# Performance work log

Hardware: AMD Instinct MI355X
Metric: run time of the kernel (lower is better)

The kernel has to match this reference:

```python
import jax, jax.numpy as jnp
import numpy as np

DIM = 1024
NUM_HEADS = 16
HEAD_DIM = DIM // NUM_HEADS


def setup_inputs() -> dict:
    key = jax.random.key(0)
    ks = jax.random.split(key, 5)
    B, T = 2, 2048
    x = jax.random.normal(ks[0], (B, T, DIM), dtype=jnp.float32)
    s = 1.0 / np.sqrt(DIM)
    W_qkv = jax.random.normal(ks[1], (DIM, 3 * DIM), dtype=jnp.float32) * s
    b_qkv = jnp.zeros((3 * DIM,), dtype=jnp.float32)
    W_out = jax.random.normal(ks[2], (DIM, DIM), dtype=jnp.float32) * s
    b_out = jnp.zeros((DIM,), dtype=jnp.float32)
    return {"x": x, "W_qkv": W_qkv, "b_qkv": b_qkv, "W_out": W_out, "b_out": b_out}


def reference(x, W_qkv, b_qkv, W_out, b_out):
    B, T, D = x.shape
    H, Hd = NUM_HEADS, HEAD_DIM
    qkv = x @ W_qkv + b_qkv                       # [B,T,3D]
    qkv = qkv.reshape(B, T, 3, H, Hd)
    q = jnp.transpose(qkv[:, :, 0], (0, 2, 1, 3))  # [B,H,T,Hd]
    k = jnp.transpose(qkv[:, :, 1], (0, 2, 1, 3))
    v = jnp.transpose(qkv[:, :, 2], (0, 2, 1, 3))
    att = jnp.einsum('bhqd,bhkd->bhqk', q, k) / np.sqrt(Hd)  # [B,H,T,T]
    causal = jnp.tril(jnp.ones((T, T), dtype=bool))
    att = jnp.where(causal[None, None], att, -jnp.inf)
    att = jax.nn.softmax(att, axis=-1)
    out = jnp.einsum('bhqk,bhkd->bhqd', att, v)   # [B,H,T,Hd]
    out = jnp.transpose(out, (0, 2, 1, 3)).reshape(B, T, D)
    return out @ W_out + b_out
```

## Files before the change

kernel.cpp:

```cpp
#include <hip/hip_runtime.h>
#include <hip/hip_bf16.h>

typedef unsigned short u16;
typedef __attribute__((ext_vector_type(8))) short short8;
typedef __attribute__((ext_vector_type(4))) float f32x4;
typedef __attribute__((ext_vector_type(4))) unsigned short u16x4;

#define LOG2E 1.44269504088896340736f


__device__ __forceinline__ void gl_lds16(const void* g, void* l) {
  __builtin_amdgcn_global_load_lds(
      (__attribute__((address_space(1))) void*)g,
      (__attribute__((address_space(3))) void*)l, 16, 0, 0);
}

__device__ __forceinline__ float exp2_fast(float x) {
#if __has_builtin(__builtin_amdgcn_exp2f)
  return __builtin_amdgcn_exp2f(x);
#else
  return exp2f(x);
#endif
}

__device__ __forceinline__ u16 f2bf(float f) {
  union { float f; unsigned int i; } v;
  v.f = f;
  unsigned int r = v.i + 0x7fffu + ((v.i >> 16) & 1u);
  return (u16)(r >> 16);
}

__device__ __forceinline__ unsigned int pack_bf2(float lo, float hi) {
  union { __hip_bfloat162 h2; unsigned int u; } c;
  c.h2 = __float22bfloat162_rn(make_float2(lo, hi));
  return c.u;
}


__global__ __launch_bounds__(256) void prep_kernel(
    const float4* __restrict__ x, u16x4* __restrict__ xb,
    const float* __restrict__ Wqkv, u16* __restrict__ WqkvT,
    const float* __restrict__ Wout, u16* __restrict__ WoutT) {
  __shared__ u16 t[64][65];
  int bid = blockIdx.x, tid = threadIdx.x;
  if (bid < 4096) {
    int i = bid * 256 + tid;
    float4 v = x[i];
    u16x4 o;
    o.x = f2bf(v.x); o.y = f2bf(v.y); o.z = f2bf(v.z); o.w = f2bf(v.w);
    xb[i] = o;
    return;
  }
  const float* W;
  u16* WT;
  int K = 1024, N, bxx, byy;
  if (bid < 4864) {
    int tt = bid - 4096;
    W = Wqkv; WT = WqkvT; N = 3072; bxx = tt % 48; byy = tt / 48;
  } else {
    int tt = bid - 4864;
    W = Wout; WT = WoutT; N = 1024; bxx = tt % 16; byy = tt / 16;
  }
  int r0 = byy * 64, c0 = bxx * 64;
  int tx = tid & 63, ty = tid >> 6;
  for (int r = ty; r < 64; r += 4)
    t[r][tx] = f2bf(W[(size_t)(r0 + r) * N + c0 + tx]);
  __syncthreads();
  for (int r = ty; r < 64; r += 4)
    WT[(size_t)(c0 + r) * K + r0 + tx] = t[tx][r];
}


template <bool OUT_F32, int BN>
__global__ __launch_bounds__(256) void gemm_bt_kernel(
    const u16* __restrict__ A, const u16* __restrict__ Bt,
    const float* __restrict__ bias, void* __restrict__ Cout,
    int M, int N, int K) {
  constexpr int NBJ = BN / 32;
  constexpr int CH_A = 16;
  constexpr int CH_B = BN / 8;
  constexpr int PER_W = (CH_A + CH_B) / 4;
  __shared__ u16 As[128 * 64];
  __shared__ u16 Bs[BN * 64];
  int tid = threadIdx.x;
  int w = tid >> 6, lane = tid & 63, l15 = lane & 15, quad = lane >> 4;
  int m0 = blockIdx.y * 128, n0 = blockIdx.x * BN;
  int wm = (w & 1) * 64, wn = (w >> 1) * (BN / 2);

  f32x4 acc[4][NBJ];
#pragma unroll
  for (int i = 0; i < 4; ++i)
#pragma unroll
    for (int j = 0; j < NBJ; ++j) {
      f32x4 z = {0.f, 0.f, 0.f, 0.f};
      acc[i][j] = z;
    }

  int r8 = lane >> 3;
  int sw = ((lane & 7) ^ r8) * 8;

  for (int kt = 0; kt < K; kt += 64) {
    __syncthreads();
#pragma unroll
    for (int i = 0; i < PER_W; ++i) {
      int c = w * PER_W + i;
      if (c < CH_A) {
        int row = m0 + c * 8 + r8;
        gl_lds16(A + (size_t)row * K + kt + sw, As + c * 512);
      } else {
        int cc = c - CH_A;
        int row = n0 + cc * 8 + r8;
        gl_lds16(Bt + (size_t)row * K + kt + sw, Bs + cc * 512);
      }
    }
    __syncthreads();

#pragma unroll
    for (int kh = 0; kh < 2; ++kh) {
      short8 af[4], bf[NBJ];
#pragma unroll
      for (int i = 0; i < 4; ++i) {
        int R = wm + i * 16 + l15;
        af[i] = *(const short8*)(As + R * 64 +
                                 ((kh * 32 + quad * 8) ^ ((R & 7) * 8)));
      }
#pragma unroll
      for (int j = 0; j < NBJ; ++j) {
        int R = wn + j * 16 + l15;
        bf[j] = *(const short8*)(Bs + R * 64 +
                                 ((kh * 32 + quad * 8) ^ ((R & 7) * 8)));
      }
#pragma unroll
      for (int i = 0; i < 4; ++i)
#pragma unroll
        for (int j = 0; j < NBJ; ++j)
          acc[i][j] = __builtin_amdgcn_mfma_f32_16x16x32_bf16(af[i], bf[j],
                                                              acc[i][j], 0, 0, 0);
    }
  }

  float bv[NBJ];
#pragma unroll
  for (int j = 0; j < NBJ; ++j) bv[j] = bias[n0 + wn + j * 16 + l15];
#pragma unroll
  for (int i = 0; i < 4; ++i)
#pragma unroll
    for (int j = 0; j < NBJ; ++j) {
      int col = n0 + wn + j * 16 + l15;
#pragma unroll
      for (int r = 0; r < 4; ++r) {
        int row = m0 + wm + i * 16 + quad * 4 + r;
        float val = acc[i][j][r] + bv[j];
        if (OUT_F32)
          ((float*)Cout)[(size_t)row * N + col] = val;
        else
          ((u16*)Cout)[(size_t)row * N + col] = f2bf(val);
      }
    }
}


__global__ __launch_bounds__(512, 2) void flash_kernel(
    const u16* __restrict__ qkv, u16* __restrict__ att) {
  __shared__ unsigned int SH[28672];

  int tid = threadIdx.x;
  int w = tid >> 6, half = w >> 2, wq = w & 3;
  int lane = tid & 63, l15 = lane & 15, quad = lane >> 4;
  int bx = blockIdx.x;
  int p = bx >> 5, bh = bx & 31, b = bh >> 4, h = bh & 15;
  const int qs[2] = {15 - p, p};
  const int kmax0 = 2 * qs[0] + 1, kmax1 = 2 * p + 1;
  const int jmax = 16 - p;

  const u16* base = qkv + (size_t)b * 2048 * 3072 + h * 64;
  const u16* kb = base + 1024;
  const u16* vb = base + 2048;

  int ht = tid & 255;
  const int krow = ht >> 3, h7 = ht & 7;
  const int swk = (h7 ^ (krow & 7)) * 8;

  short8 qf[2][2][2];
#pragma unroll
  for (int t = 0; t < 2; ++t) {
    const u16* qtb = base + (size_t)(qs[t] * 128 + wq * 32 + l15) * 3072;
    qf[t][0][0] = *(const short8*)(qtb + quad * 8);
    qf[t][0][1] = *(const short8*)(qtb + 32 + quad * 8);
    qf[t][1][0] = *(const short8*)(qtb + 16 * 3072 + quad * 8);
    qf[t][1][1] = *(const short8*)(qtb + 16 * 3072 + 32 + quad * 8);
  }

  {
    unsigned int* Ks0 = SH + half * 2048;
    gl_lds16(kb + (size_t)(half * 64 + krow) * 3072 + swk,
             (char*)Ks0 + wq * 1024);
    gl_lds16(kb + (size_t)(half * 64 + 32 + krow) * 3072 + swk,
             (char*)Ks0 + 4096 + wq * 1024);
  }
  uint4 vr0 = *(const uint4*)(vb + (size_t)(half * 64 + 2 * krow) * 3072 + h7 * 8);
  uint4 vr1 = *(const uint4*)(vb + (size_t)(half * 64 + 2 * krow + 1) * 3072 + h7 * 8);

  f32x4 o[2][2][4];
#pragma unroll
  for (int t = 0; t < 2; ++t)
#pragma unroll
    for (int qsub = 0; qsub < 2; ++qsub)
#pragma unroll
      for (int jd = 0; jd < 4; ++jd) {
        f32x4 z = {0.f, 0.f, 0.f, 0.f};
        o[t][qsub][jd] = z;
      }
  float lsum[2][2] = {0.f, 0.f, 0.f, 0.f};

  const int psw = (l15 & 7) << 2;
  const float kscale = 0.125f * LOG2E;
  unsigned int* Pw = SH + 20480 + w * 1024;

  int b3 = 0;
  for (int j = 0; j < jmax; ++j) {
    int kt = 2 * j + half;
    unsigned int* KsH = SH + b3 * 4096 + half * 2048;
    unsigned int* VtH = SH + 12288 + (j & 1) * 4096 + half * 2048;

    {
      const u16* av = (const u16*)&vr0;
      const u16* bvp = (const u16*)&vr1;
#pragma unroll
      for (int jj = 0; jj < 8; ++jj) {
        int d = h7 * 8 + jj;
        VtH[32 * d + (krow ^ ((jj ^ h7) << 2))] =
            (unsigned int)av[jj] | ((unsigned int)bvp[jj] << 16);
      }
    }

    int nb3 = b3 + 1;
    if (nb3 == 3) nb3 = 0;
    if (j + 1 < jmax) {
      int kn = (kt + 2) * 64;
      unsigned int* Ksn = SH + nb3 * 4096 + half * 2048;
      gl_lds16(kb + (size_t)(kn + krow) * 3072 + swk, (char*)Ksn + wq * 1024);
      gl_lds16(kb + (size_t)(kn + 32 + krow) * 3072 + swk,
               (char*)Ksn + 4096 + wq * 1024);
      vr0 = *(const uint4*)(vb + (size_t)(kn + 2 * krow) * 3072 + h7 * 8);
      vr1 = *(const uint4*)(vb + (size_t)(kn + 2 * krow + 1) * 3072 + h7 * 8);
    }
    b3 = nb3;

    asm volatile("s_waitcnt lgkmcnt(0)" ::: "memory");
    __builtin_amdgcn_s_barrier();
    asm volatile("" ::: "memory");

#pragma unroll
    for (int t = 0; t < 2; ++t) {
      int km = t ? kmax1 : kmax0;
      if (kt > km) continue;
      bool last = (kt == km);
      if (last && wq < 2) continue;
      bool domask = last || ((kt == km - 1) && wq < 2);
      int qloc = ((last ? (wq - 2) : wq) << 5) + l15;

      f32x4 s0[4], s1[4];
#pragma unroll
      for (int jn = 0; jn < 4; ++jn) {
        f32x4 z = {0.f, 0.f, 0.f, 0.f};
        s0[jn] = z;
        s1[jn] = z;
      }
#pragma unroll
      for (int ss = 0; ss < 2; ++ss) {
        short8 a0 = qf[t][0][ss];
        short8 a1 = qf[t][1][ss];
#pragma unroll
        for (int jn = 0; jn < 4; ++jn) {
          int row = jn * 16 + l15;
          short8 bk = *(const short8*)&KsH[32 * row + ((16 * ss + 4 * quad) ^
                                                       ((row & 7) << 2))];
          s0[jn] = __builtin_amdgcn_mfma_f32_16x16x32_bf16(bk, a0, s0[jn], 0, 0, 0);
          s1[jn] = __builtin_amdgcn_mfma_f32_16x16x32_bf16(bk, a1, s1[jn], 0, 0, 0);
        }
      }

#pragma unroll
      for (int qsub = 0; qsub < 2; ++qsub) {
        int qq = qloc + qsub * 16;
        float ls = 0.f;
#pragma unroll
        for (int jn = 0; jn < 4; ++jn) {
          f32x4 sv = qsub ? s1[jn] : s0[jn];
          float pv[4];
#pragma unroll
          for (int r = 0; r < 4; ++r) {
            float e = exp2_fast(fmaf(sv[r], kscale, -16.0f));
            if (domask && (jn * 16 + quad * 4 + r > qq)) e = 0.f;
            pv[r] = e;
            ls += e;
          }
          uint2 dd = make_uint2(pack_bf2(pv[0], pv[1]), pack_bf2(pv[2], pv[3]));
          *(uint2*)&Pw[qsub * 512 + 32 * l15 +
                       (((jn << 3) + (quad << 1)) ^ psw)] = dd;
        }
        lsum[t][qsub] += ls;
      }

#pragma unroll
      for (int ss = 0; ss < 2; ++ss) {
        short8 pf0 = *(const short8*)&Pw[32 * l15 +
                                         (((ss << 4) + (quad << 2)) ^ psw)];
        short8 pf1 = *(const short8*)&Pw[512 + 32 * l15 +
                                         (((ss << 4) + (quad << 2)) ^ psw)];
#pragma unroll
        for (int jd = 0; jd < 4; ++jd) {
          int vrow = jd * 16 + l15;
          int f = (vrow & 7) ^ ((vrow >> 3) & 7);
          short8 bvv = *(const short8*)&VtH[32 * vrow +
                                            (((ss << 4) + (quad << 2)) ^ (f << 2))];
          o[t][0][jd] =
              __builtin_amdgcn_mfma_f32_16x16x32_bf16(bvv, pf0, o[t][0][jd], 0, 0, 0);
          o[t][1][jd] =
              __builtin_amdgcn_mfma_f32_16x16x32_bf16(bvv, pf1, o[t][1][jd], 0, 0, 0);
        }
      }
    }
  }

  float lf[2][2];
#pragma unroll
  for (int t = 0; t < 2; ++t)
#pragma unroll
    for (int qsub = 0; qsub < 2; ++qsub) {
      float v = lsum[t][qsub];
      v += __shfl_xor(v, 16, 64);
      v += __shfl_xor(v, 32, 64);
      lf[t][qsub] = v;
    }

  float* OM = (float*)SH;
  float* LM = (float*)(SH + 8704);
  __syncthreads();
#pragma unroll
  for (int t = 0; t < 2; ++t) {
    if (half == 0) {
#pragma unroll
      for (int qsub = 0; qsub < 2; ++qsub) {
        int q = wq * 32 + qsub * 16 + l15;
#pragma unroll
        for (int jd = 0; jd < 4; ++jd)
          *(float4*)&OM[q * 68 + jd * 16 + quad * 4] = *(float4*)&o[t][qsub][jd];
        if (quad == 0) LM[q] = lf[t][qsub];
      }
    }
    __syncthreads();
    if (half == 1) {
#pragma unroll
      for (int qsub = 0; qsub < 2; ++qsub) {
        int q = wq * 32 + qsub * 16 + l15;
        float lr = lf[t][qsub] + LM[q];
        float inv = 1.f / lr;
        size_t row = (size_t)b * 2048 + qs[t] * 128 + q;
        u16* orow = att + row * 1024 + h * 64 + quad * 4;
#pragma unroll
        for (int jd = 0; jd < 4; ++jd) {
          float4 pa = *(float4*)&OM[q * 68 + jd * 16 + quad * 4];
          uint2 dd = make_uint2(pack_bf2((o[t][qsub][jd][0] + pa.x) * inv,
                                         (o[t][qsub][jd][1] + pa.y) * inv),
                                pack_bf2((o[t][qsub][jd][2] + pa.z) * inv,
                                         (o[t][qsub][jd][3] + pa.w) * inv));
          *(uint2*)(orow + jd * 16) = dd;
        }
      }
    }
    __syncthreads();
  }
}


extern "C" void kernel_launch(void* const* d_in, const int* in_sizes, int n_in,
                              void* d_out, int out_size, void* d_ws,
                              size_t ws_size, hipStream_t stream) {
  const float* x = (const float*)d_in[0];
  const float* Wqkv = (const float*)d_in[1];
  const float* bqkv = (const float*)d_in[2];
  const float* Wout = (const float*)d_in[3];
  const float* bout = (const float*)d_in[4];
  float* out = (float*)d_out;

  char* ws = (char*)d_ws;
  u16* WqkvT = (u16*)(ws);
  u16* WoutT = (u16*)(ws + 6291456);
  u16* qkv = (u16*)(ws + 8388608);
  u16* attn = (u16*)(ws + 33554432);
  u16* xb = (u16*)(ws + 41943040);

  prep_kernel<<<5120, 256, 0, stream>>>((const float4*)x, (u16x4*)xb, Wqkv,
                                        WqkvT, Wout, WoutT);
  gemm_bt_kernel<false, 128><<<dim3(24, 32), 256, 0, stream>>>(
      xb, WqkvT, bqkv, (void*)qkv, 4096, 3072, 1024);
  flash_kernel<<<256, 512, 0, stream>>>(qkv, attn);
  gemm_bt_kernel<true, 64><<<dim3(16, 32), 256, 0, stream>>>(
      attn, WoutT, bout, (void*)out, 4096, 1024, 1024);
}
```

Baseline: 169.4 us.

## Use 256x256-tile 8-wave GEMM kernel for QKV projection

Adds a new GEMM kernel with 256x256 output tiles, 8 waves each computing 128x64, and double-buffered LDS filled by direct global-to-LDS loads with XOR swizzle. It is used for the QKV projection in place of the 128-wide tile kernel. Larger tiles raise data reuse and cut global traffic per FLOP. The cost is a grid of only 192 blocks on a GPU with many CUs, one block per CU, and a full vmcnt(0) wait plus barrier every K step, which limits latency hiding.

```diff
diff --git a/kernel.cpp b/kernel.cpp
--- a/kernel.cpp
+++ b/kernel.cpp
@@ -160,6 +160,101 @@
 }
 
 
+template <bool OUT_F32>
+__global__ __launch_bounds__(512, 1) void gemm8_kernel(
+    const u16* __restrict__ A, const u16* __restrict__ Bt,
+    const float* __restrict__ bias, void* __restrict__ Cout,
+    int M, int N, int K) {
+  __shared__ u16 LDS[2][2][256 * 64];
+  int tid = threadIdx.x;
+  int w = tid >> 6, lane = tid & 63, l15 = lane & 15, quad = lane >> 4;
+  int m0 = blockIdx.y * 256, n0 = blockIdx.x * 256;
+  int wm = (w & 1) * 128, wn = (w >> 1) * 64;
+
+  f32x4 acc[8][4];
+#pragma unroll
+  for (int i = 0; i < 8; ++i)
+#pragma unroll
+    for (int j = 0; j < 4; ++j) {
+      f32x4 z = {0.f, 0.f, 0.f, 0.f};
+      acc[i][j] = z;
+    }
+
+  int r8 = lane >> 3;
+  int sw = ((lane & 7) ^ r8) * 8;
+
+  const u16* Asrc = A + (size_t)(m0 + w * 32 + r8) * K + sw;
+  const u16* Bsrc = Bt + (size_t)(n0 + w * 32 + r8) * K + sw;
+  int nt = K >> 6;
+
+#pragma unroll
+  for (int i = 0; i < 4; ++i) {
+    gl_lds16(Asrc + (size_t)(i * 8) * K, &LDS[0][0][(w * 4 + i) * 512]);
+    gl_lds16(Bsrc + (size_t)(i * 8) * K, &LDS[0][1][(w * 4 + i) * 512]);
+  }
+
+  for (int t = 0; t < nt; ++t) {
+    asm volatile("s_waitcnt vmcnt(0)" ::: "memory");
+    __builtin_amdgcn_s_barrier();
+    asm volatile("" ::: "memory");
+    int cur = t & 1;
+    if (t + 1 < nt) {
+      int koff = (t + 1) << 6;
+#pragma unroll
+      for (int i = 0; i < 4; ++i) {
+        gl_lds16(Asrc + (size_t)(i * 8) * K + koff,
+                 &LDS[cur ^ 1][0][(w * 4 + i) * 512]);
+        gl_lds16(Bsrc + (size_t)(i * 8) * K + koff,
+                 &LDS[cur ^ 1][1][(w * 4 + i) * 512]);
+      }
+    }
+    const u16* As = &LDS[cur][0][0];
+    const u16* Bs = &LDS[cur][1][0];
+#pragma unroll
+    for (int kh = 0; kh < 2; ++kh) {
+      short8 af[8], bf[4];
+#pragma unroll
+      for (int i = 0; i < 8; ++i) {
+        int R = wm + i * 16 + l15;
+        af[i] = *(const short8*)(As + R * 64 +
+                                 ((kh * 32 + quad * 8) ^ ((R & 7) * 8)));
+      }
+#pragma unroll
+      for (int j = 0; j < 4; ++j) {
+        int R = wn + j * 16 + l15;
+        bf[j] = *(const short8*)(Bs + R * 64 +
+                                 ((kh * 32 + quad * 8) ^ ((R & 7) * 8)));
+      }
+#pragma unroll
+      for (int i = 0; i < 8; ++i)
+#pragma unroll
+        for (int j = 0; j < 4; ++j)
+          acc[i][j] = __builtin_amdgcn_mfma_f32_16x16x32_bf16(af[i], bf[j],
+                                                              acc[i][j], 0, 0, 0);
+    }
+  }
+
+  float bv[4];
+#pragma unroll
+  for (int j = 0; j < 4; ++j) bv[j] = bias[n0 + wn + j * 16 + l15];
+#pragma unroll
+  for (int i = 0; i < 8; ++i)
+#pragma unroll
+    for (int j = 0; j < 4; ++j) {
+      int col = n0 + wn + j * 16 + l15;
+#pragma unroll
+      for (int r = 0; r < 4; ++r) {
+        int row = m0 + wm + i * 16 + quad * 4 + r;
+        float val = acc[i][j][r] + bv[j];
+        if (OUT_F32)
+          ((float*)Cout)[(size_t)row * N + col] = val;
+        else
+          ((u16*)Cout)[(size_t)row * N + col] = f2bf(val);
+      }
+    }
+}
+
+
 __global__ __launch_bounds__(512, 2) void flash_kernel(
     const u16* __restrict__ qkv, u16* __restrict__ att) {
   __shared__ unsigned int SH[28672];
@@ -394,7 +489,7 @@
 
   prep_kernel<<<5120, 256, 0, stream>>>((const float4*)x, (u16x4*)xb, Wqkv,
                                         WqkvT, Wout, WoutT);
-  gemm_bt_kernel<false, 128><<<dim3(24, 32), 256, 0, stream>>>(
+  gemm8_kernel<false><<<dim3(12, 16), 512, 0, stream>>>(
       xb, WqkvT, bqkv, (void*)qkv, 4096, 3072, 1024);
   flash_kernel<<<256, 512, 0, stream>>>(qkv, attn);
   gemm_bt_kernel<true, 64><<<dim3(16, 32), 256, 0, stream>>>(
```

After: 173.2 us. 2.3% more time.

## Double-buffer GEMM LDS loads with 8-wave blocks and larger tiles

Applied to the files above, without the earlier changes.

Replaces the 4-wave GEMM with an 8-wave kernel that double-buffers the A/B tiles in LDS. The next K-tile's global-to-LDS loads are issued before the current tile's MFMAs, and the second barrier per iteration is removed. Tiles grow to 256x192 for the QKV projection and 128x128 for the output projection, which launches 256 blocks per GEMM. This aims to hide load latency and improve data reuse, but it raises register and LDS use and may leave CUs underfilled.

```diff
diff --git a/kernel.cpp b/kernel.cpp
--- a/kernel.cpp
+++ b/kernel.cpp
@@ -71,27 +71,27 @@
 }
 
 
-template <bool OUT_F32, int BN>
-__global__ __launch_bounds__(256) void gemm_bt_kernel(
+template <bool OUT_F32, int BM, int BN>
+__global__ __launch_bounds__(512, 1) void gemm8_kernel(
     const u16* __restrict__ A, const u16* __restrict__ Bt,
     const float* __restrict__ bias, void* __restrict__ Cout,
     int M, int N, int K) {
-  constexpr int NBJ = BN / 32;
-  constexpr int CH_A = 16;
+  constexpr int MI = BM / 32;
+  constexpr int NJ = BN / 64;
+  constexpr int CH_A = BM / 8;
   constexpr int CH_B = BN / 8;
-  constexpr int PER_W = (CH_A + CH_B) / 4;
-  __shared__ u16 As[128 * 64];
-  __shared__ u16 Bs[BN * 64];
+  constexpr int PER_W = (CH_A + CH_B) / 8;
+  __shared__ u16 LDS[2][(BM + BN) * 64];
   int tid = threadIdx.x;
   int w = tid >> 6, lane = tid & 63, l15 = lane & 15, quad = lane >> 4;
-  int m0 = blockIdx.y * 128, n0 = blockIdx.x * BN;
-  int wm = (w & 1) * 64, wn = (w >> 1) * (BN / 2);
-
-  f32x4 acc[4][NBJ];
-#pragma unroll
-  for (int i = 0; i < 4; ++i)
-#pragma unroll
-    for (int j = 0; j < NBJ; ++j) {
+  int m0 = blockIdx.y * BM, n0 = blockIdx.x * BN;
+  int wm = (w & 1) * (BM / 2), wn = (w >> 1) * (BN / 4);
+
+  f32x4 acc[MI][NJ];
+#pragma unroll
+  for (int i = 0; i < MI; ++i)
+#pragma unroll
+    for (int j = 0; j < NJ; ++j) {
       f32x4 z = {0.f, 0.f, 0.f, 0.f};
       acc[i][j] = z;
     }
@@ -99,53 +99,67 @@
   int r8 = lane >> 3;
   int sw = ((lane & 7) ^ r8) * 8;
 
-  for (int kt = 0; kt < K; kt += 64) {
-    __syncthreads();
-#pragma unroll
-    for (int i = 0; i < PER_W; ++i) {
-      int c = w * PER_W + i;
-      if (c < CH_A) {
-        int row = m0 + c * 8 + r8;
-        gl_lds16(A + (size_t)row * K + kt + sw, As + c * 512);
-      } else {
-        int cc = c - CH_A;
-        int row = n0 + cc * 8 + r8;
-        gl_lds16(Bt + (size_t)row * K + kt + sw, Bs + cc * 512);
-      }
-    }
-    __syncthreads();
-
+  const u16* srcp[PER_W];
+  int dsto[PER_W];
+#pragma unroll
+  for (int i = 0; i < PER_W; ++i) {
+    int c = w * PER_W + i;
+    if (c < CH_A) {
+      srcp[i] = A + (size_t)(m0 + c * 8 + r8) * K + sw;
+    } else {
+      srcp[i] = Bt + (size_t)(n0 + (c - CH_A) * 8 + r8) * K + sw;
+    }
+    dsto[i] = c * 512;
+  }
+
+  int nt = K >> 6;
+#pragma unroll
+  for (int i = 0; i < PER_W; ++i) gl_lds16(srcp[i], &LDS[0][dsto[i]]);
+
+  for (int t = 0; t < nt; ++t) {
+    asm volatile("s_waitcnt vmcnt(0)" ::: "memory");
+    __builtin_amdgcn_s_barrier();
+    asm volatile("" ::: "memory");
+    int cur = t & 1;
+    if (t + 1 < nt) {
+      int koff = (t + 1) << 6;
+#pragma unroll
+      for (int i = 0; i < PER_W; ++i)
+        gl_lds16(srcp[i] + koff, &LDS[cur ^ 1][dsto[i]]);
+    }
+    const u16* As = &LDS[cur][0];
+    const u16* Bs = &LDS[cur][CH_A * 512];
 #pragma unroll
     for (int kh = 0; kh < 2; ++kh) {
-      short8 af[4], bf[NBJ];
-#pragma unroll
-      for (int i = 0; i < 4; ++i) {
+      short8 af[MI], bf[NJ];
+#pragma unroll
+      for (int i = 0; i < MI; ++i) {
         int R = wm + i * 16 + l15;
         af[i] = *(const short8*)(As + R * 64 +
                                  ((kh * 32 + quad * 8) ^ ((R & 7) * 8)));
       }
 #pragma unroll
-      for (int j = 0; j < NBJ; ++j) {
+      for (int j = 0; j < NJ; ++j) {
         int R = wn + j * 16 + l15;
         bf[j] = *(const short8*)(Bs + R * 64 +
                                  ((kh * 32 + quad * 8) ^ ((R & 7) * 8)));
       }
 #pragma unroll
-      for (int i = 0; i < 4; ++i)
-#pragma unroll
-        for (int j = 0; j < NBJ; ++j)
+      for (int i = 0; i < MI; ++i)
+#pragma unroll
+        for (int j = 0; j < NJ; ++j)
           acc[i][j] = __builtin_amdgcn_mfma_f32_16x16x32_bf16(af[i], bf[j],
                                                               acc[i][j], 0, 0, 0);
     }
   }
 
-  float bv[NBJ];
-#pragma unroll
-  for (int j = 0; j < NBJ; ++j) bv[j] = bias[n0 + wn + j * 16 + l15];
-#pragma unroll
-  for (int i = 0; i < 4; ++i)
-#pragma unroll
-    for (int j = 0; j < NBJ; ++j) {
+  float bv[NJ];
+#pragma unroll
+  for (int j = 0; j < NJ; ++j) bv[j] = bias[n0 + wn + j * 16 + l15];
+#pragma unroll
+  for (int i = 0; i < MI; ++i)
+#pragma unroll
+    for (int j = 0; j < NJ; ++j) {
       int col = n0 + wn + j * 16 + l15;
 #pragma unroll
       for (int r = 0; r < 4; ++r) {
@@ -394,9 +408,9 @@
 
   prep_kernel<<<5120, 256, 0, stream>>>((const float4*)x, (u16x4*)xb, Wqkv,
                                         WqkvT, Wout, WoutT);
-  gemm_bt_kernel<false, 128><<<dim3(24, 32), 256, 0, stream>>>(
+  gemm8_kernel<false, 256, 192><<<dim3(16, 16), 512, 0, stream>>>(
       xb, WqkvT, bqkv, (void*)qkv, 4096, 3072, 1024);
   flash_kernel<<<256, 512, 0, stream>>>(qkv, attn);
-  gemm_bt_kernel<true, 64><<<dim3(16, 32), 256, 0, stream>>>(
+  gemm8_kernel<true, 128, 128><<<dim3(8, 32), 512, 0, stream>>>(
       attn, WoutT, bout, (void*)out, 4096, 1024, 1024);
 }
```

Result: no change. 167.0 us (-1.4%).
